# Kernel tuning notes

Hardware: AMD Instinct MI355X
Metric: run time of the kernel (lower is better)

The kernel has to match this reference:

```python
import jax, jax.numpy as jnp
import numpy as np

D = 1024
DFF = 4096
B, S = 4, 2048
EPS = 1e-6
SLOPE = 0.01  # torch LeakyReLU default


def setup_inputs() -> dict:
    key = jax.random.key(0)
    ks = jax.random.split(key, 16)
    sd = 1.0 / np.sqrt(D)
    sf = 1.0 / np.sqrt(DFF)
    return {
        "X": jax.random.normal(ks[0], (B, S, D), dtype=jnp.float32),
        "intensity": jax.random.uniform(ks[1], (B, S, S), dtype=jnp.float32),
        "Wq": jax.random.uniform(ks[2], (D, D), jnp.float32, -sd, sd),
        "bq": jax.random.uniform(ks[3], (D,), jnp.float32, -sd, sd),
        "Wk": jax.random.uniform(ks[4], (D, D), jnp.float32, -sd, sd),
        "bk": jax.random.uniform(ks[5], (D,), jnp.float32, -sd, sd),
        "Wv": jax.random.uniform(ks[6], (D, D), jnp.float32, -sd, sd),
        "bv": jax.random.uniform(ks[7], (D,), jnp.float32, -sd, sd),
        "Wo": jax.random.uniform(ks[8], (D, D), jnp.float32, -sd, sd),
        "bo": jax.random.uniform(ks[9], (D,), jnp.float32, -sd, sd),
        "W1": jax.random.uniform(ks[10], (D, DFF), jnp.float32, -sd, sd),
        "b1": jax.random.uniform(ks[11], (DFF,), jnp.float32, -sd, sd),
        "W2": jax.random.uniform(ks[12], (DFF, D), jnp.float32, -sf, sf),
        "b2": jax.random.uniform(ks[13], (D,), jnp.float32, -sf, sf),
        "g1": jnp.ones((D,), jnp.float32),
        "be1": jnp.zeros((D,), jnp.float32),
        "g2": jnp.ones((D,), jnp.float32),
        "be2": jnp.zeros((D,), jnp.float32),
    }


def _layernorm(x, g, b):
    mu = jnp.mean(x, axis=-1, keepdims=True)
    var = jnp.mean(jnp.square(x - mu), axis=-1, keepdims=True)
    return (x - mu) * jax.lax.rsqrt(var + EPS) * g + b


def reference(X, intensity, Wq, bq, Wk, bk, Wv, bv, Wo, bo, W1, b1, W2, b2, g1, be1, g2, be2):
    d_k = X.shape[-1]
    q = X @ Wq + bq
    k = X @ Wk + bk
    v = X @ Wv + bv
    # scores: [B,S,S]; scale applied to k^T as in source
    scores = jnp.einsum('bid,bjd->bij', q, k) / jnp.sqrt(jnp.float32(d_k))
    attn = jax.nn.softmax(scores, axis=-1) + intensity  # post-softmax bias add
    out = jnp.einsum('bij,bjd->bid', attn, v) @ Wo + bo
    h = _layernorm(out + X, g1, be1)
    ffn = jax.nn.leaky_relu(h @ W1 + b1, negative_slope=SLOPE) @ W2 + b2
    return _layernorm(ffn + h, g2, be2)
```

## Files before the change

kernel.cpp:

```cpp
#include <hip/hip_runtime.h>

#define B_   4
#define S_   2048
#define D_   1024
#define DFF_ 4096

typedef __attribute__((ext_vector_type(8))) short short8;
typedef __attribute__((ext_vector_type(4))) float floatx4;

__device__ __forceinline__ unsigned short f2b(float f) {
    unsigned int u = __float_as_uint(f);
    unsigned int r = (u + 0x7fffu + ((u >> 16) & 1u)) >> 16;
    return (unsigned short)r;
}
__device__ __forceinline__ float b2f(unsigned short u) {
    return __uint_as_float((unsigned int)u << 16);
}

__device__ __forceinline__ void swizzle_xy(int gx, int gy, int& bx, int& by) {
    if ((gy & 7) == 0) {
        const int linear = by * gx + bx;
        const int xcd = linear & 7;
        const int slot = linear >> 3;
        const int r = slot / gx;
        by = xcd * (gy >> 3) + r;
        bx = slot - r * gx;
    }
}

__device__ __forceinline__ void gemm_core256(
    const unsigned short* __restrict__ A,
    const unsigned short* __restrict__ Bt,
    int ldA, int ldB, int K, int m0, int n0,
    unsigned short* As, unsigned short* Bs,
    floatx4 acc[4][4])
{
    const int tid  = threadIdx.x;
    const int lane = tid & 63;
    const int wave = tid >> 6;

    const int ra = tid >> 3;
    const int pg = tid & 7;
    const int cg = (pg ^ (ra & 7)) * 8;
    const unsigned short* gA = A  + (long long)(m0 + ra) * ldA + cg;
    const unsigned short* gB = Bt + (long long)(n0 + ra) * ldB + cg;
    const long long pA = 64LL * ldA;
    const long long pB = 64LL * ldB;

    unsigned short* dA = As + wave * 512;
    unsigned short* dB = Bs + wave * 512;

    const int wr = (wave >> 1) * 64;
    const int wc = (wave & 1) * 64;
    const int fr = lane & 15;
    const int q  = lane >> 4;

    int aoff[2][4], boff[2][4];
#pragma unroll
    for (int h = 0; h < 2; h++)
#pragma unroll
        for (int i = 0; i < 4; i++) {
            const int rA = wr + i * 16 + fr;
            const int rB = wc + i * 16 + fr;
            const int g  = h * 4 + q;
            aoff[h][i] = rA * 64 + ((g ^ (rA & 7)) * 8);
            boff[h][i] = rB * 64 + ((g ^ (rB & 7)) * 8);
        }

    for (int k0 = 0; k0 < K; k0 += 64) {
        __syncthreads();
#pragma unroll
        for (int p = 0; p < 4; p++)
            __builtin_amdgcn_global_load_lds(
                (const __attribute__((address_space(1))) void*)(gA + k0 + p * pA),
                (__attribute__((address_space(3))) void*)(dA + p * 4096), 16, 0, 0);
#pragma unroll
        for (int p = 0; p < 2; p++)
            __builtin_amdgcn_global_load_lds(
                (const __attribute__((address_space(1))) void*)(gB + k0 + p * pB),
                (__attribute__((address_space(3))) void*)(dB + p * 4096), 16, 0, 0);
        __syncthreads();

#pragma unroll
        for (int h = 0; h < 2; h++) {
            short8 af[4], bfr[4];
#pragma unroll
            for (int mi = 0; mi < 4; mi++) af[mi] = *(const short8*)&As[aoff[h][mi]];
#pragma unroll
            for (int ni = 0; ni < 4; ni++) bfr[ni] = *(const short8*)&Bs[boff[h][ni]];
#pragma unroll
            for (int mi = 0; mi < 4; mi++)
#pragma unroll
                for (int ni = 0; ni < 4; ni++)
                    acc[mi][ni] = __builtin_amdgcn_mfma_f32_16x16x32_bf16(
                        af[mi], bfr[ni], acc[mi][ni], 0, 0, 0);
        }
    }
}

__global__ __launch_bounds__(256) void cast_bf16_kernel(
    const float4* __restrict__ src, ushort4* __restrict__ dst, int n4)
{
    int i = blockIdx.x * 256 + threadIdx.x;
    if (i < n4) {
        float4 f = src[i];
        ushort4 u;
        u.x = f2b(f.x); u.y = f2b(f.y); u.z = f2b(f.z); u.w = f2b(f.w);
        dst[i] = u;
    }
}

__global__ __launch_bounds__(256) void transpose_cast_kernel(
    const float* __restrict__ W, unsigned short* __restrict__ Wt, int K, int N)
{
    __shared__ float tile[32][33];
    const int tx = threadIdx.x;
    const int ty = threadIdx.y;
    const int bx = blockIdx.x * 32;
    const int by = blockIdx.y * 32;
#pragma unroll
    for (int j = 0; j < 32; j += 8)
        tile[ty + j][tx] = W[(long long)(by + ty + j) * N + bx + tx];
    __syncthreads();
#pragma unroll
    for (int j = 0; j < 32; j += 8)
        Wt[(long long)(bx + ty + j) * K + by + tx] = f2b(tile[tx][ty + j]);
}

template <int OUT_BF16, int ACT_LEAKY, int HAS_BIAS>
__global__ __launch_bounds__(512, 4) void gemm_bt(
    const unsigned short* __restrict__ A,
    const unsigned short* __restrict__ Bt,
    void* __restrict__ Cptr,
    const float* __restrict__ bias,
    int M, int N, int K, float scale,
    long long sA, long long sB, long long sC)
{
    __shared__ unsigned short As[256 * 64];
    __shared__ unsigned short Bs[128 * 64];

    const int lane = threadIdx.x & 63;
    const int wave = threadIdx.x >> 6;
    const int z    = blockIdx.z;

    int bx = blockIdx.x, by = blockIdx.y;
    swizzle_xy(gridDim.x, gridDim.y, bx, by);
    const int m0 = by * 256;
    const int n0 = bx * 128;

    floatx4 acc[4][4];
#pragma unroll
    for (int i = 0; i < 4; i++)
#pragma unroll
        for (int j = 0; j < 4; j++) acc[i][j] = floatx4{0.f, 0.f, 0.f, 0.f};

    gemm_core256(A + (long long)z * sA, Bt + (long long)z * sB,
                 K, K, K, m0, n0, As, Bs, acc);

    const int wr = (wave >> 1) * 64;
    const int wc = (wave & 1) * 64;
    const int cr = (lane >> 4) * 4;
    const int cc = lane & 15;
    float* Cf = (float*)Cptr;
    unsigned short* Cb = (unsigned short*)Cptr;

#pragma unroll
    for (int mi = 0; mi < 4; mi++) {
#pragma unroll
        for (int ni = 0; ni < 4; ni++) {
            const int col = n0 + wc + ni * 16 + cc;
            const float bv = HAS_BIAS ? bias[col] : 0.0f;
#pragma unroll
            for (int r = 0; r < 4; r++) {
                const int row = m0 + wr + mi * 16 + cr + r;
                float v = acc[mi][ni][r] * scale + bv;
                if (ACT_LEAKY) v = (v > 0.0f) ? v : 0.01f * v;
                const long long idx = (long long)z * sC + (long long)row * N + col;
                if (OUT_BF16) Cb[idx] = f2b(v); else Cf[idx] = v;
            }
        }
    }
}

template <int NK, int PBF16>
__global__ __launch_bounds__(512, 4) void gemm_bt_sk(
    const unsigned short* __restrict__ A,
    const unsigned short* __restrict__ Bt,
    void* __restrict__ Pptr,
    int M, int N, int Kslice, int ldA, int ldB,
    long long sA, long long sB)
{
    __shared__ unsigned short As[256 * 64];
    __shared__ unsigned short Bs[128 * 64];

    const int lane = threadIdx.x & 63;
    const int wave = threadIdx.x >> 6;
    const int z    = blockIdx.z;
    const int ks   = z % NK;
    const int b    = z / NK;
    const int nb   = gridDim.z / NK;

    int bx = blockIdx.x, by = blockIdx.y;
    swizzle_xy(gridDim.x, gridDim.y, bx, by);
    const int m0 = by * 256;
    const int n0 = bx * 128;

    floatx4 acc[4][4];
#pragma unroll
    for (int i = 0; i < 4; i++)
#pragma unroll
        for (int j = 0; j < 4; j++) acc[i][j] = floatx4{0.f, 0.f, 0.f, 0.f};

    gemm_core256(A + (long long)b * sA + (long long)ks * Kslice,
                 Bt + (long long)b * sB + (long long)ks * Kslice,
                 ldA, ldB, Kslice, m0, n0, As, Bs, acc);

    const long long pbase = ((long long)ks * nb + b) * (long long)M * N;

    const int wr = (wave >> 1) * 64;
    const int wc = (wave & 1) * 64;
    const int cr = (lane >> 4) * 4;
    const int cc = lane & 15;
    float* Pf = (float*)Pptr;
    unsigned short* Ph = (unsigned short*)Pptr;

#pragma unroll
    for (int mi = 0; mi < 4; mi++) {
#pragma unroll
        for (int ni = 0; ni < 4; ni++) {
            const int col = n0 + wc + ni * 16 + cc;
#pragma unroll
            for (int r = 0; r < 4; r++) {
                const int row = m0 + wr + mi * 16 + cr + r;
                const long long idx = pbase + (long long)row * N + col;
                if (PBF16) Ph[idx] = f2b(acc[mi][ni][r]);
                else       Pf[idx] = acc[mi][ni][r];
            }
        }
    }
}

__global__ __launch_bounds__(512, 4) void gemm_qkv(
    const unsigned short* __restrict__ A,
    const unsigned short* __restrict__ Bt,
    unsigned short* __restrict__ Qb,
    unsigned short* __restrict__ Kb,
    unsigned short* __restrict__ Vt,
    const float* __restrict__ bq,
    const float* __restrict__ bk,
    const float* __restrict__ bv)
{
    __shared__ unsigned short As[256 * 64];
    __shared__ unsigned short Bs[128 * 64];

    const int lane = threadIdx.x & 63;
    const int wave = threadIdx.x >> 6;

    int bx = blockIdx.x, by = blockIdx.y;
    swizzle_xy(gridDim.x, gridDim.y, bx, by);
    const int m0 = by * 256;
    const int n0 = bx * 128;

    floatx4 acc[4][4];
#pragma unroll
    for (int i = 0; i < 4; i++)
#pragma unroll
        for (int j = 0; j < 4; j++) acc[i][j] = floatx4{0.f, 0.f, 0.f, 0.f};

    gemm_core256(A, Bt, D_, D_, D_, m0, n0, As, Bs, acc);

    const int wr = (wave >> 1) * 64;
    const int wc = (wave & 1) * 64;
    const int cr = (lane >> 4) * 4;
    const int cc = lane & 15;

#pragma unroll
    for (int mi = 0; mi < 4; mi++) {
#pragma unroll
        for (int ni = 0; ni < 4; ni++) {
            const int col = n0 + wc + ni * 16 + cc;
            const int seg = col >> 10;
            const int c = col & 1023;
            const float* bp = (seg == 0) ? bq : ((seg == 1) ? bk : bv);
            const float bval = bp[c];
#pragma unroll
            for (int r = 0; r < 4; r++) {
                const int row = m0 + wr + mi * 16 + cr + r;
                const unsigned short o = f2b(acc[mi][ni][r] + bval);
                if (seg == 0) {
                    Qb[(long long)row * D_ + c] = o;
                } else if (seg == 1) {
                    Kb[(long long)row * D_ + c] = o;
                } else {
                    const int b = row >> 11;
                    const int s = row & (S_ - 1);
                    Vt[((long long)b * D_ + c) * S_ + s] = o;
                }
            }
        }
    }
}

__global__ __launch_bounds__(256) void avred_kernel(
    const ushort4* __restrict__ p0, const ushort4* __restrict__ p1,
    ushort4* __restrict__ dst, int n4)
{
    int i = blockIdx.x * 256 + threadIdx.x;
    if (i < n4) {
        ushort4 a = p0[i], b = p1[i];
        ushort4 u;
        u.x = f2b(b2f(a.x) + b2f(b.x)); u.y = f2b(b2f(a.y) + b2f(b.y));
        u.z = f2b(b2f(a.z) + b2f(b.z)); u.w = f2b(b2f(a.w) + b2f(b.w));
        dst[i] = u;
    }
}

template <int HAS_OUTB>
__global__ __launch_bounds__(256) void ln_red_kernel(
    const float* __restrict__ p0, const float* __restrict__ p1,
    const float* __restrict__ resid, const float* __restrict__ bias,
    const float* __restrict__ g, const float* __restrict__ b,
    float* __restrict__ out_f, unsigned short* __restrict__ out_b)
{
    __shared__ float red[8];
    const long long row = blockIdx.x;
    const int tid = threadIdx.x;
    const float4 a0 = ((const float4*)(p0 + row * D_))[tid];
    const float4 a1 = ((const float4*)(p1 + row * D_))[tid];
    const float4 rv = ((const float4*)(resid + row * D_))[tid];
    const float4 bi = ((const float4*)bias)[tid];
    float v0 = a0.x + a1.x + bi.x + rv.x;
    float v1 = a0.y + a1.y + bi.y + rv.y;
    float v2 = a0.z + a1.z + bi.z + rv.z;
    float v3 = a0.w + a1.w + bi.w + rv.w;

    float s = v0 + v1 + v2 + v3;
#pragma unroll
    for (int o = 32; o > 0; o >>= 1) s += __shfl_xor(s, o);
    if ((tid & 63) == 0) red[tid >> 6] = s;
    __syncthreads();
    const float mean = (red[0] + red[1] + red[2] + red[3]) * (1.0f / D_);

    const float d0 = v0 - mean, d1 = v1 - mean, d2 = v2 - mean, d3 = v3 - mean;
    float q = d0 * d0 + d1 * d1 + d2 * d2 + d3 * d3;
#pragma unroll
    for (int o = 32; o > 0; o >>= 1) q += __shfl_xor(q, o);
    if ((tid & 63) == 0) red[4 + (tid >> 6)] = q;
    __syncthreads();
    const float var = (red[4] + red[5] + red[6] + red[7]) * (1.0f / D_);
    const float inv = rsqrtf(var + 1e-6f);

    const float4 gv = ((const float4*)g)[tid];
    const float4 bv = ((const float4*)b)[tid];
    const float o0 = d0 * inv * gv.x + bv.x;
    const float o1 = d1 * inv * gv.y + bv.y;
    const float o2 = d2 * inv * gv.z + bv.z;
    const float o3 = d3 * inv * gv.w + bv.w;

    ((float4*)(out_f + row * D_))[tid] = float4{o0, o1, o2, o3};
    if (HAS_OUTB) {
        ushort4 u; u.x = f2b(o0); u.y = f2b(o1); u.z = f2b(o2); u.w = f2b(o3);
        ((ushort4*)(out_b + row * D_))[tid] = u;
    }
}

__global__ __launch_bounds__(256) void softmax_bias_kernel(
    const unsigned short* __restrict__ scores, const float* __restrict__ intensity,
    unsigned short* __restrict__ attn)
{
    __shared__ float red[8];
    const long long row = blockIdx.x;
    const int tid = threadIdx.x;
    const ushort4* s4 = (const ushort4*)(scores + row * S_);
    const float4* i4 = (const float4*)(intensity + row * S_);
    ushort4* dst = (ushort4*)(attn + row * S_);

    float vv[8];
    {
        ushort4 a = s4[tid], b = s4[tid + 256];
        vv[0] = b2f(a.x); vv[1] = b2f(a.y); vv[2] = b2f(a.z); vv[3] = b2f(a.w);
        vv[4] = b2f(b.x); vv[5] = b2f(b.y); vv[6] = b2f(b.z); vv[7] = b2f(b.w);
    }

    float mx = vv[0];
#pragma unroll
    for (int i = 1; i < 8; i++) mx = fmaxf(mx, vv[i]);
#pragma unroll
    for (int o = 32; o > 0; o >>= 1) mx = fmaxf(mx, __shfl_xor(mx, o));
    if ((tid & 63) == 0) red[tid >> 6] = mx;
    __syncthreads();
    mx = fmaxf(fmaxf(red[0], red[1]), fmaxf(red[2], red[3]));

    float e[8];
    float sum = 0.f;
#pragma unroll
    for (int i = 0; i < 8; i++) { e[i] = __expf(vv[i] - mx); sum += e[i]; }
#pragma unroll
    for (int o = 32; o > 0; o >>= 1) sum += __shfl_xor(sum, o);
    if ((tid & 63) == 0) red[4 + (tid >> 6)] = sum;
    __syncthreads();
    sum = red[4] + red[5] + red[6] + red[7];
    const float rs = 1.0f / sum;

#pragma unroll
    for (int i = 0; i < 2; i++) {
        float4 iv = i4[tid + 256 * i];
        ushort4 o;
        o.x = f2b(e[4 * i + 0] * rs + iv.x);
        o.y = f2b(e[4 * i + 1] * rs + iv.y);
        o.z = f2b(e[4 * i + 2] * rs + iv.z);
        o.w = f2b(e[4 * i + 3] * rs + iv.w);
        dst[tid + 256 * i] = o;
    }
}

extern "C" void kernel_launch(void* const* d_in, const int* in_sizes, int n_in,
                              void* d_out, int out_size, void* d_ws, size_t ws_size,
                              hipStream_t stream)
{
    const float* X   = (const float*)d_in[0];
    const float* inten = (const float*)d_in[1];
    const float* Wq  = (const float*)d_in[2];
    const float* bq  = (const float*)d_in[3];
    const float* Wk  = (const float*)d_in[4];
    const float* bk  = (const float*)d_in[5];
    const float* Wv  = (const float*)d_in[6];
    const float* bv  = (const float*)d_in[7];
    const float* Wo  = (const float*)d_in[8];
    const float* bo  = (const float*)d_in[9];
    const float* W1  = (const float*)d_in[10];
    const float* b1  = (const float*)d_in[11];
    const float* W2  = (const float*)d_in[12];
    const float* b2  = (const float*)d_in[13];
    const float* g1  = (const float*)d_in[14];
    const float* be1 = (const float*)d_in[15];
    const float* g2  = (const float*)d_in[16];
    const float* be2 = (const float*)d_in[17];
    float* out = (float*)d_out;

    char* ws = (char*)d_ws;
    const size_t MB = 1ull << 20;
    unsigned short* Xb   = (unsigned short*)(ws + 0);
    unsigned short* Wqkv = (unsigned short*)(ws + 16 * MB);
    unsigned short* Wot  = (unsigned short*)(ws + 22 * MB);
    unsigned short* W1t  = (unsigned short*)(ws + 24 * MB);
    unsigned short* W2t  = (unsigned short*)(ws + 32 * MB);
    unsigned short* Qb   = (unsigned short*)(ws + 40 * MB);
    unsigned short* Kb   = (unsigned short*)(ws + 56 * MB);
    unsigned short* Vt   = (unsigned short*)(ws + 72 * MB);
    unsigned short* Sc   = (unsigned short*)(ws + 88 * MB);
    unsigned short* At   = (unsigned short*)(ws + 152 * MB);
    unsigned short* AVp  = (unsigned short*)(ws + 88 * MB);
    unsigned short* AVb  = (unsigned short*)(ws + 0);
    float*          Op   = (float*)(ws + 152 * MB);
    float*          Hf   = (float*)(ws + 40 * MB);
    unsigned short* Hb   = (unsigned short*)(ws + 72 * MB);
    unsigned short* F1   = (unsigned short*)(ws + 88 * MB);
    float*          Fp   = (float*)(ws + 152 * MB);

    const dim3 blk(256);
    const dim3 blk512(512);
    const dim3 tblk(32, 8);
    const long long MN_d = (long long)B_ * S_ * D_;

    cast_bf16_kernel<<<dim3(8192), blk, 0, stream>>>(
        (const float4*)X, (ushort4*)Xb, B_ * S_ * D_ / 4);
    transpose_cast_kernel<<<dim3(D_ / 32, D_ / 32), tblk, 0, stream>>>(
        Wq, Wqkv, D_, D_);
    transpose_cast_kernel<<<dim3(D_ / 32, D_ / 32), tblk, 0, stream>>>(
        Wk, Wqkv + 1024 * 1024, D_, D_);
    transpose_cast_kernel<<<dim3(D_ / 32, D_ / 32), tblk, 0, stream>>>(
        Wv, Wqkv + 2048 * 1024, D_, D_);
    transpose_cast_kernel<<<dim3(D_ / 32, D_ / 32), tblk, 0, stream>>>(Wo, Wot, D_, D_);
    transpose_cast_kernel<<<dim3(DFF_ / 32, D_ / 32), tblk, 0, stream>>>(W1, W1t, D_, DFF_);
    transpose_cast_kernel<<<dim3(D_ / 32, DFF_ / 32), tblk, 0, stream>>>(W2, W2t, DFF_, D_);

    gemm_qkv<<<dim3(24, 32), blk512, 0, stream>>>(Xb, Wqkv, Qb, Kb, Vt, bq, bk, bv);

    gemm_bt<1, 0, 0><<<dim3(16, 8, 4), blk512, 0, stream>>>(
        Qb, Kb, Sc, nullptr, S_, S_, D_, 0.03125f,
        (long long)S_ * D_, (long long)S_ * D_, (long long)S_ * S_);

    softmax_bias_kernel<<<dim3(B_ * S_), blk, 0, stream>>>(Sc, inten, At);

    gemm_bt_sk<2, 1><<<dim3(8, 8, 8), blk512, 0, stream>>>(
        At, Vt, AVp, S_, D_, S_ / 2, S_, S_,
        (long long)S_ * S_, (long long)D_ * S_);
    avred_kernel<<<dim3(8192), blk, 0, stream>>>(
        (const ushort4*)AVp, (const ushort4*)(AVp + MN_d), (ushort4*)AVb,
        (int)(MN_d / 4));

    gemm_bt_sk<2, 0><<<dim3(8, 32, 2), blk512, 0, stream>>>(
        AVb, Wot, Op, B_ * S_, D_, D_ / 2, D_, D_, 0, 0);

    ln_red_kernel<1><<<dim3(B_ * S_), blk, 0, stream>>>(
        Op, Op + MN_d, X, bo, g1, be1, Hf, Hb);

    gemm_bt<1, 1, 1><<<dim3(32, 32), blk512, 0, stream>>>(
        Hb, W1t, F1, b1, B_ * S_, DFF_, D_, 1.0f, 0, 0, 0);

    gemm_bt_sk<2, 0><<<dim3(8, 32, 2), blk512, 0, stream>>>(
        F1, W2t, Fp, B_ * S_, D_, DFF_ / 2, DFF_, DFF_, 0, 0);

    ln_red_kernel<0><<<dim3(B_ * S_), blk, 0, stream>>>(
        Fp, Fp + MN_d, Hf, b2, g2, be2, out, nullptr);
}
```

Baseline: 576.3 us.

## Write V row-major and transpose separately; store split-K partials in bf16

The QKV GEMM epilogue now writes V in row-major layout, which avoids the strided scattered stores of the old transposed write. A new tiled LDS transpose kernel then builds Vt. Split-K partial outputs for the Wo and W2 GEMMs are stored as bf16 instead of fp32, which halves partial write and read traffic in the layernorm-reduce kernels. The cost is an extra kernel launch plus one more pass over V, and reduced precision on the partial sums.

Measured after the change: 560.1 us. 2.8% less time.

```diff
diff --git a/kernel.cpp b/kernel.cpp
--- a/kernel.cpp
+++ b/kernel.cpp
@@ -127,6 +127,40 @@
         Wt[(long long)(bx + ty + j) * K + by + tx] = f2b(tile[tx][ty + j]);
 }
 
+__global__ __launch_bounds__(256) void vtrans_kernel(
+    const unsigned short* __restrict__ Vb, unsigned short* __restrict__ Vt)
+{
+    __shared__ unsigned short tile[64][68];
+    const int b  = blockIdx.z;
+    const int s0 = blockIdx.y * 64;
+    const int d0 = blockIdx.x * 64;
+    const int tx = threadIdx.x & 15;
+    const int ty = threadIdx.x >> 4;
+
+    const unsigned short* src = Vb + ((long long)b * S_ + s0) * D_ + d0;
+#pragma unroll
+    for (int j = 0; j < 4; j++) {
+        const int s = j * 16 + ty;
+        ushort4 v = *(const ushort4*)(src + (long long)s * D_ + tx * 4);
+        tile[tx * 4 + 0][s] = v.x;
+        tile[tx * 4 + 1][s] = v.y;
+        tile[tx * 4 + 2][s] = v.z;
+        tile[tx * 4 + 3][s] = v.w;
+    }
+    __syncthreads();
+    unsigned short* dst = Vt + ((long long)b * D_ + d0) * S_ + s0;
+#pragma unroll
+    for (int j = 0; j < 4; j++) {
+        const int d = j * 16 + ty;
+        ushort4 v;
+        v.x = tile[d][tx * 4 + 0];
+        v.y = tile[d][tx * 4 + 1];
+        v.z = tile[d][tx * 4 + 2];
+        v.w = tile[d][tx * 4 + 3];
+        *(ushort4*)(dst + (long long)d * S_ + tx * 4) = v;
+    }
+}
+
 template <int OUT_BF16, int ACT_LEAKY, int HAS_BIAS>
 __global__ __launch_bounds__(512, 4) void gemm_bt(
     const unsigned short* __restrict__ A,
@@ -182,11 +216,11 @@
     }
 }
 
-template <int NK, int PBF16>
+template <int NK>
 __global__ __launch_bounds__(512, 4) void gemm_bt_sk(
     const unsigned short* __restrict__ A,
     const unsigned short* __restrict__ Bt,
-    void* __restrict__ Pptr,
+    unsigned short* __restrict__ P,
     int M, int N, int Kslice, int ldA, int ldB,
     long long sA, long long sB)
 {
@@ -221,8 +255,6 @@
     const int wc = (wave & 1) * 64;
     const int cr = (lane >> 4) * 4;
     const int cc = lane & 15;
-    float* Pf = (float*)Pptr;
-    unsigned short* Ph = (unsigned short*)Pptr;
 
 #pragma unroll
     for (int mi = 0; mi < 4; mi++) {
@@ -232,9 +264,7 @@
 #pragma unroll
             for (int r = 0; r < 4; r++) {
                 const int row = m0 + wr + mi * 16 + cr + r;
-                const long long idx = pbase + (long long)row * N + col;
-                if (PBF16) Ph[idx] = f2b(acc[mi][ni][r]);
-                else       Pf[idx] = acc[mi][ni][r];
+                P[pbase + (long long)row * N + col] = f2b(acc[mi][ni][r]);
             }
         }
     }
@@ -245,7 +275,7 @@
     const unsigned short* __restrict__ Bt,
     unsigned short* __restrict__ Qb,
     unsigned short* __restrict__ Kb,
-    unsigned short* __restrict__ Vt,
+    unsigned short* __restrict__ Vb,
     const float* __restrict__ bq,
     const float* __restrict__ bk,
     const float* __restrict__ bv)
@@ -282,20 +312,12 @@
             const int seg = col >> 10;
             const int c = col & 1023;
             const float* bp = (seg == 0) ? bq : ((seg == 1) ? bk : bv);
+            unsigned short* dp = (seg == 0) ? Qb : ((seg == 1) ? Kb : Vb);
             const float bval = bp[c];
 #pragma unroll
             for (int r = 0; r < 4; r++) {
                 const int row = m0 + wr + mi * 16 + cr + r;
-                const unsigned short o = f2b(acc[mi][ni][r] + bval);
-                if (seg == 0) {
-                    Qb[(long long)row * D_ + c] = o;
-                } else if (seg == 1) {
-                    Kb[(long long)row * D_ + c] = o;
-                } else {
-                    const int b = row >> 11;
-                    const int s = row & (S_ - 1);
-                    Vt[((long long)b * D_ + c) * S_ + s] = o;
-                }
+                dp[(long long)row * D_ + c] = f2b(acc[mi][ni][r] + bval);
             }
         }
     }
@@ -317,7 +339,7 @@
 
 template <int HAS_OUTB>
 __global__ __launch_bounds__(256) void ln_red_kernel(
-    const float* __restrict__ p0, const float* __restrict__ p1,
+    const unsigned short* __restrict__ p0, const unsigned short* __restrict__ p1,
     const float* __restrict__ resid, const float* __restrict__ bias,
     const float* __restrict__ g, const float* __restrict__ b,
     float* __restrict__ out_f, unsigned short* __restrict__ out_b)
@@ -325,14 +347,14 @@
     __shared__ float red[8];
     const long long row = blockIdx.x;
     const int tid = threadIdx.x;
-    const float4 a0 = ((const float4*)(p0 + row * D_))[tid];
-    const float4 a1 = ((const float4*)(p1 + row * D_))[tid];
+    const ushort4 a0 = ((const ushort4*)(p0 + row * D_))[tid];
+    const ushort4 a1 = ((const ushort4*)(p1 + row * D_))[tid];
     const float4 rv = ((const float4*)(resid + row * D_))[tid];
     const float4 bi = ((const float4*)bias)[tid];
-    float v0 = a0.x + a1.x + bi.x + rv.x;
-    float v1 = a0.y + a1.y + bi.y + rv.y;
-    float v2 = a0.z + a1.z + bi.z + rv.z;
-    float v3 = a0.w + a1.w + bi.w + rv.w;
+    float v0 = b2f(a0.x) + b2f(a1.x) + bi.x + rv.x;
+    float v1 = b2f(a0.y) + b2f(a1.y) + bi.y + rv.y;
+    float v2 = b2f(a0.z) + b2f(a1.z) + bi.z + rv.z;
+    float v3 = b2f(a0.w) + b2f(a1.w) + bi.w + rv.w;
 
     float s = v0 + v1 + v2 + v3;
 #pragma unroll
@@ -449,14 +471,15 @@
     unsigned short* Kb   = (unsigned short*)(ws + 56 * MB);
     unsigned short* Vt   = (unsigned short*)(ws + 72 * MB);
     unsigned short* Sc   = (unsigned short*)(ws + 88 * MB);
+    unsigned short* Vb   = (unsigned short*)(ws + 152 * MB);
     unsigned short* At   = (unsigned short*)(ws + 152 * MB);
     unsigned short* AVp  = (unsigned short*)(ws + 88 * MB);
     unsigned short* AVb  = (unsigned short*)(ws + 0);
-    float*          Op   = (float*)(ws + 152 * MB);
+    unsigned short* Op   = (unsigned short*)(ws + 152 * MB);
     float*          Hf   = (float*)(ws + 40 * MB);
     unsigned short* Hb   = (unsigned short*)(ws + 72 * MB);
     unsigned short* F1   = (unsigned short*)(ws + 88 * MB);
-    float*          Fp   = (float*)(ws + 152 * MB);
+    unsigned short* Fp   = (unsigned short*)(ws + 152 * MB);
 
     const dim3 blk(256);
     const dim3 blk512(512);
@@ -475,7 +498,9 @@
     transpose_cast_kernel<<<dim3(DFF_ / 32, D_ / 32), tblk, 0, stream>>>(W1, W1t, D_, DFF_);
     transpose_cast_kernel<<<dim3(D_ / 32, DFF_ / 32), tblk, 0, stream>>>(W2, W2t, DFF_, D_);
 
-    gemm_qkv<<<dim3(24, 32), blk512, 0, stream>>>(Xb, Wqkv, Qb, Kb, Vt, bq, bk, bv);
+    gemm_qkv<<<dim3(24, 32), blk512, 0, stream>>>(Xb, Wqkv, Qb, Kb, Vb, bq, bk, bv);
+
+    vtrans_kernel<<<dim3(D_ / 64, S_ / 64, B_), blk, 0, stream>>>(Vb, Vt);
 
     gemm_bt<1, 0, 0><<<dim3(16, 8, 4), blk512, 0, stream>>>(
         Qb, Kb, Sc, nullptr, S_, S_, D_, 0.03125f,
@@ -483,14 +508,14 @@
 
     softmax_bias_kernel<<<dim3(B_ * S_), blk, 0, stream>>>(Sc, inten, At);
 
-    gemm_bt_sk<2, 1><<<dim3(8, 8, 8), blk512, 0, stream>>>(
+    gemm_bt_sk<2><<<dim3(8, 8, 8), blk512, 0, stream>>>(
         At, Vt, AVp, S_, D_, S_ / 2, S_, S_,
         (long long)S_ * S_, (long long)D_ * S_);
     avred_kernel<<<dim3(8192), blk, 0, stream>>>(
         (const ushort4*)AVp, (const ushort4*)(AVp + MN_d), (ushort4*)AVb,
         (int)(MN_d / 4));
 
-    gemm_bt_sk<2, 0><<<dim3(8, 32, 2), blk512, 0, stream>>>(
+    gemm_bt_sk<2><<<dim3(8, 32, 2), blk512, 0, stream>>>(
         AVb, Wot, Op, B_ * S_, D_, D_ / 2, D_, D_, 0, 0);
 
     ln_red_kernel<1><<<dim3(B_ * S_), blk, 0, stream>>>(
@@ -499,7 +524,7 @@
     gemm_bt<1, 1, 1><<<dim3(32, 32), blk512, 0, stream>>>(
         Hb, W1t, F1, b1, B_ * S_, DFF_, D_, 1.0f, 0, 0, 0);
 
-    gemm_bt_sk<2, 0><<<dim3(8, 32, 2), blk512, 0, stream>>>(
+    gemm_bt_sk<2><<<dim3(8, 32, 2), blk512, 0, stream>>>(
         F1, W2t, Fp, B_ * S_, D_, DFF_ / 2, DFF_, DFF_, 0, 0);
 
     ln_red_kernel<0><<<dim3(B_ * S_), blk, 0, stream>>>(
```
